# Kernel optimization log

Hardware: AMD Instinct MI355X
Metric: run time of the kernel (lower is better)

## Reference

```python
import jax, jax.numpy as jnp
import numpy as np
from jax.scipy.special import logsumexp

EPS = 0.1
MAX_ITER = 100
LOG_SHIFT = 1e-8


def setup_inputs() -> dict:
    key = jax.random.key(0)
    kx, ky = jax.random.split(key)
    x = jax.random.normal(kx, (4, 2048, 64), dtype=jnp.float32)
    y = jax.random.normal(ky, (4, 2048, 64), dtype=jnp.float32)
    return {"x": x, "y": y}


def _cost_matrix(x, y):
    # |x_i - y_j|^2 summed over features; for p=2 use the expanded quadratic form
    # to avoid materializing a [B, P1, P2, D] intermediate.
    x2 = jnp.sum(x * x, axis=-1)  # [B, P1]
    y2 = jnp.sum(y * y, axis=-1)  # [B, P2]
    xy = jnp.einsum('bpd,bqd->bpq', x, y)  # [B, P1, P2]
    return x2[:, :, None] + y2[:, None, :] - 2.0 * xy


def _M(C, u, v):
    # M_ij = (-C_ij + u_i + v_j) / eps
    return (-C + u[..., :, None] + v[..., None, :]) / EPS


def reference(x, y):
    C = _cost_matrix(x, y)  # [B, P1, P2]
    B, P1, P2 = C.shape
    mu = jnp.full((B, P1), 1.0 / P1, dtype=C.dtype)
    nu = jnp.full((B, P2), 1.0 / P2, dtype=C.dtype)
    log_mu = jnp.log(mu + LOG_SHIFT)
    log_nu = jnp.log(nu + LOG_SHIFT)

    def step(carry, _):
        u, v = carry
        u = EPS * (log_mu - logsumexp(_M(C, u, v), axis=-1)) + u
        # logsumexp of M^T over its last dim == logsumexp of M over axis -2
        v = EPS * (log_nu - logsumexp(_M(C, u, v), axis=-2)) + v
        return (u, v), None

    u0 = jnp.zeros_like(mu)
    v0 = jnp.zeros_like(nu)
    (u, v), _ = jax.lax.scan(step, (u0, v0), None, length=MAX_ITER)

    pi = jnp.exp(_M(C, u, v))  # transport plan [B, P1, P2]
    cost = jnp.sum(pi * C, axis=(-2, -1))  # [B], reduction='none'
    return cost, pi, C
```

## Files before the change

### kernel.cpp

```cpp
#include <hip/hip_runtime.h>
#include <hip/hip_bf16.h>
#include <math.h>


#define P 2048
#define D 64
#define B 4
#define ITERS 100
#define EPS 0.1f
#define KS 14.426950408889634f
#define EL2 0.06931471805599453f

#define EX2 __builtin_amdgcn_exp2f
#define LG2 __builtin_amdgcn_logf

__global__ __launch_bounds__(256) void cost_kernel(
    const float* __restrict__ X, const float* __restrict__ Y,
    float* __restrict__ C) {
  __shared__ float xs[64][65];
  __shared__ float ys[64][65];
  const int b = blockIdx.z;
  const int i0 = blockIdx.y * 64;
  const int j0 = blockIdx.x * 64;
  const float* Xb = X + ((size_t)b * P + i0) * D;
  const float* Yb = Y + ((size_t)b * P + j0) * D;
  const int t = threadIdx.x;
#pragma unroll
  for (int n = 0; n < 4; n++) {
    int e4 = t + n * 256;
    float4 xv = ((const float4*)Xb)[e4];
    float4 yv = ((const float4*)Yb)[e4];
    int r = e4 >> 4;
    int k = (e4 & 15) * 4;
    xs[r][k] = xv.x; xs[r][k + 1] = xv.y; xs[r][k + 2] = xv.z; xs[r][k + 3] = xv.w;
    ys[r][k] = yv.x; ys[r][k + 1] = yv.y; ys[r][k + 2] = yv.z; ys[r][k + 3] = yv.w;
  }
  __syncthreads();
  const int tx = t & 15;
  const int ty = t >> 4;
  float acc[4][4] = {};
#pragma unroll
  for (int k = 0; k < D; k++) {
    float a[4], bb[4];
#pragma unroll
    for (int r = 0; r < 4; r++) a[r] = xs[ty * 4 + r][k];
#pragma unroll
    for (int c = 0; c < 4; c++) bb[c] = ys[tx * 4 + c][k];
#pragma unroll
    for (int r = 0; r < 4; r++)
#pragma unroll
      for (int c = 0; c < 4; c++) {
        float d = a[r] - bb[c];
        acc[r][c] = fmaf(d, d, acc[r][c]);
      }
  }
#pragma unroll
  for (int r = 0; r < 4; r++) {
    float4 o = make_float4(acc[r][0], acc[r][1], acc[r][2], acc[r][3]);
    *(float4*)&C[((size_t)b * P + i0 + ty * 4 + r) * P + j0 + tx * 4] = o;
  }
}

__global__ __launch_bounds__(256, 3) void sweep8(
    const float* __restrict__ C, const float* __restrict__ vK,
    float* __restrict__ uK, float2* __restrict__ part, float elogK) {
  const int bid = blockIdx.x;
  const int rows0 = bid * 8;
  const int b = bid >> 8;
  const int kb = bid & 255;
  const int t = threadIdx.x;
  const int lane = t & 63;
  const int w = t >> 6;

  __shared__ float redm[4][8];
  __shared__ float reds[4][8];

  float vv[8];
  {
    const float4* vp = (const float4*)(vK + ((size_t)b << 11) + t * 8);
    float4 a = vp[0], q = vp[1];
    vv[0] = a.x; vv[1] = a.y; vv[2] = a.z; vv[3] = a.w;
    vv[4] = q.x; vv[5] = q.y; vv[6] = q.z; vv[7] = q.w;
  }

  float cK[8][8];
  {
    const float* Cb = C + (size_t)rows0 * P + t * 8;
#pragma unroll
    for (int r = 0; r < 8; r++) {
      float4 a = *(const float4*)(Cb + (size_t)r * P);
      float4 q = *(const float4*)(Cb + (size_t)r * P + 4);
      cK[r][0] = a.x * KS; cK[r][1] = a.y * KS; cK[r][2] = a.z * KS; cK[r][3] = a.w * KS;
      cK[r][4] = q.x * KS; cK[r][5] = q.y * KS; cK[r][6] = q.z * KS; cK[r][7] = q.w * KS;
    }
  }

  float bm[8];
#pragma unroll
  for (int r = 0; r < 8; r++) {
    float m = vv[0] - cK[r][0];
#pragma unroll
    for (int j = 1; j < 8; j++) m = fmaxf(m, vv[j] - cK[r][j]);
#pragma unroll
    for (int off = 32; off; off >>= 1) m = fmaxf(m, __shfl_xor(m, off));
    bm[r] = m;
  }
  if (lane == 0) {
#pragma unroll
    for (int r = 0; r < 8; r++) redm[w][r] = bm[r];
  }
  __syncthreads();
#pragma unroll
  for (int r = 0; r < 8; r++)
    bm[r] = fmaxf(fmaxf(redm[0][r], redm[1][r]),
                  fmaxf(redm[2][r], redm[3][r]));
  float ls[8];
#pragma unroll
  for (int r = 0; r < 8; r++) {
    float s = 0.f;
#pragma unroll
    for (int j = 0; j < 8; j++) s += EX2(vv[j] - cK[r][j] - bm[r]);
#pragma unroll
    for (int off = 32; off; off >>= 1) s += __shfl_xor(s, off);
    ls[r] = s;
  }
  if (lane == 0) {
#pragma unroll
    for (int r = 0; r < 8; r++) reds[w][r] = ls[r];
  }
  __syncthreads();
  float ur[8];
#pragma unroll
  for (int r = 0; r < 8; r++) {
    float S = (reds[0][r] + reds[1][r]) + (reds[2][r] + reds[3][r]);
    ur[r] = elogK - bm[r] - LG2(S);
  }
  if (t == 0) {
#pragma unroll
    for (int r = 0; r < 8; r++) uK[rows0 + r] = ur[r];
  }

  float4* p4 = (float4*)(part + (size_t)kb * (B * P) + ((size_t)b << 11) + t * 8);
#pragma unroll
  for (int i = 0; i < 4; i++) {
    float m0, s0, m1, s1;
    {
      const int cc = 2 * i;
      float z[8];
#pragma unroll
      for (int r = 0; r < 8; r++) z[r] = ur[r] - cK[r][cc];
      m0 = z[0];
#pragma unroll
      for (int r = 1; r < 8; r++) m0 = fmaxf(m0, z[r]);
      s0 = 0.f;
#pragma unroll
      for (int r = 0; r < 8; r++) s0 += EX2(z[r] - m0);
    }
    {
      const int cc = 2 * i + 1;
      float z[8];
#pragma unroll
      for (int r = 0; r < 8; r++) z[r] = ur[r] - cK[r][cc];
      m1 = z[0];
#pragma unroll
      for (int r = 1; r < 8; r++) m1 = fmaxf(m1, z[r]);
      s1 = 0.f;
#pragma unroll
      for (int r = 0; r < 8; r++) s1 += EX2(z[r] - m1);
    }
    p4[i] = make_float4(m0, s0, m1, s1);
  }
}

__global__ __launch_bounds__(256) void reduce_v3(
    const float2* __restrict__ part, float* __restrict__ vK, float elogK) {
  const int t = threadIdx.x;
  const int c = t & 15;
  const int seg = t >> 4;
  const int col = blockIdx.x * 16 + c;
  const float2* pk = part + (size_t)(seg * 16) * (B * P) + col;
  float m = -__builtin_inff();
  float s = 0.f;
#pragma unroll
  for (int i = 0; i < 16; i++) {
    float2 p = pk[(size_t)i * (B * P)];
    float M = fmaxf(m, p.x);
    s = s * EX2(m - M) + p.y * EX2(p.x - M);
    m = M;
  }
#pragma unroll
  for (int off = 16; off <= 32; off <<= 1) {
    float om = __shfl_xor(m, off);
    float os = __shfl_xor(s, off);
    float M = fmaxf(m, om);
    s = s * EX2(m - M) + os * EX2(om - M);
    m = M;
  }
  __shared__ float mm[4][16];
  __shared__ float ss[4][16];
  if ((t & 63) < 16) {
    mm[t >> 6][c] = m;
    ss[t >> 6][c] = s;
  }
  __syncthreads();
  if (t < 16) {
    float M0 = mm[0][t], S0 = ss[0][t];
#pragma unroll
    for (int k = 1; k < 4; k++) {
      float pm = mm[k][t], ps = ss[k][t];
      float M = fmaxf(M0, pm);
      S0 = S0 * EX2(M0 - M) + ps * EX2(pm - M);
      M0 = M;
    }
    vK[blockIdx.x * 16 + t] = elogK - M0 - LG2(S0);
  }
}

__global__ __launch_bounds__(256) void final_pi2(
    const float* __restrict__ C, const float* __restrict__ uK,
    const float* __restrict__ vK, float* __restrict__ pi,
    float* __restrict__ cost) {
  const int bid = blockIdx.x;
  const int rows0 = bid * 4;
  const int b = rows0 >> 11;
  const int t = threadIdx.x;
  const int lane = t & 63;
  const int w = t >> 6;

  float vv[8];
  {
    const float4* vp = (const float4*)(vK + ((size_t)b << 11) + t * 8);
    float4 a = vp[0], q = vp[1];
    vv[0] = a.x; vv[1] = a.y; vv[2] = a.z; vv[3] = a.w;
    vv[4] = q.x; vv[5] = q.y; vv[6] = q.z; vv[7] = q.w;
  }

  float acc = 0.f;
#pragma unroll
  for (int r = 0; r < 4; r++) {
    const int row = rows0 + r;
    const float u = uK[row];
    const float* cp = C + (size_t)row * P + t * 8;
    float4 a = *(const float4*)(cp);
    float4 q = *(const float4*)(cp + 4);
    float c[8] = {a.x, a.y, a.z, a.w, q.x, q.y, q.z, q.w};
    float p[8];
#pragma unroll
    for (int j = 0; j < 8; j++) {
      p[j] = EX2(u + vv[j] - c[j] * KS);
      acc = fmaf(p[j], c[j], acc);
    }
    float* pp = pi + (size_t)row * P + t * 8;
    *(float4*)(pp) = make_float4(p[0], p[1], p[2], p[3]);
    *(float4*)(pp + 4) = make_float4(p[4], p[5], p[6], p[7]);
  }
#pragma unroll
  for (int off = 32; off; off >>= 1) acc += __shfl_xor(acc, off);
  __shared__ float sa[4];
  if (lane == 0) sa[w] = acc;
  __syncthreads();
  if (t == 0) atomicAdd(cost + b, (sa[0] + sa[1]) + (sa[2] + sa[3]));
}

extern "C" void kernel_launch(void* const* d_in, const int* in_sizes, int n_in,
                              void* d_out, int out_size, void* d_ws,
                              size_t ws_size, hipStream_t stream) {
  const float* x = (const float*)d_in[0];
  const float* y = (const float*)d_in[1];
  float* out = (float*)d_out;
  float* cost = out;
  float* pi = out + 4;
  float* Cmat = out + 4 + (size_t)B * P * P;

  float2* part = (float2*)pi;
  float* vK = (float*)d_ws;
  float* uK = vK + B * P;

  hipMemsetAsync(vK, 0, B * P * sizeof(float), stream);
  hipMemsetAsync(cost, 0, 4 * sizeof(float), stream);

  dim3 cgrid(P / 64, P / 64, B);
  cost_kernel<<<cgrid, 256, 0, stream>>>(x, y, Cmat);

  const float elogK = log2f(1.0f / (float)P + 1e-8f);

  for (int it = 0; it < ITERS; it++) {
    sweep8<<<B * P / 8, 256, 0, stream>>>(Cmat, vK, uK, part, elogK);
    reduce_v3<<<B * P / 16, 256, 0, stream>>>(part, vK, elogK);
  }

  final_pi2<<<B * P / 4, 256, 0, stream>>>(Cmat, uK, vK, pi, cost);
}
```

Baseline: 2.713 ms.

## Use a transposed cost matrix so both Sinkhorn half-steps are row sweeps

Builds a second, transposed cost matrix in the pi output buffer. Each iteration now runs the same row-wise logsumexp kernel twice, once on C for u and once on C^T for v. This replaces the fused row sweep that wrote partial column (max, sum) pairs and the separate reduction kernel that merged them. Each iteration reads the full matrix twice instead of once plus a large partials write and read, and the sweep uses 4 rows per block with a higher occupancy hint.

```diff
diff --git a/kernel.cpp b/kernel.cpp
--- a/kernel.cpp
+++ b/kernel.cpp
@@ -9,7 +9,6 @@
 #define ITERS 100
 #define EPS 0.1f
 #define KS 14.426950408889634f
-#define EL2 0.06931471805599453f
 
 #define EX2 __builtin_amdgcn_exp2f
 #define LG2 __builtin_amdgcn_logf
@@ -61,158 +60,78 @@
   }
 }
 
-__global__ __launch_bounds__(256, 3) void sweep8(
-    const float* __restrict__ C, const float* __restrict__ vK,
-    float* __restrict__ uK, float2* __restrict__ part, float elogK) {
+__global__ __launch_bounds__(256, 4) void lse_sweep(
+    const float* __restrict__ mat, const float* __restrict__ vin,
+    float* __restrict__ vout, float elogK) {
   const int bid = blockIdx.x;
-  const int rows0 = bid * 8;
-  const int b = bid >> 8;
-  const int kb = bid & 255;
+  const int rows0 = bid * 4;
+  const int b = rows0 >> 11;
   const int t = threadIdx.x;
   const int lane = t & 63;
   const int w = t >> 6;
 
-  __shared__ float redm[4][8];
-  __shared__ float reds[4][8];
+  __shared__ float redm[4][4];
+  __shared__ float reds[4][4];
 
   float vv[8];
   {
-    const float4* vp = (const float4*)(vK + ((size_t)b << 11) + t * 8);
+    const float4* vp = (const float4*)(vin + ((size_t)b << 11) + t * 8);
     float4 a = vp[0], q = vp[1];
     vv[0] = a.x; vv[1] = a.y; vv[2] = a.z; vv[3] = a.w;
     vv[4] = q.x; vv[5] = q.y; vv[6] = q.z; vv[7] = q.w;
   }
 
-  float cK[8][8];
+  float za[4][8];
   {
-    const float* Cb = C + (size_t)rows0 * P + t * 8;
-#pragma unroll
-    for (int r = 0; r < 8; r++) {
-      float4 a = *(const float4*)(Cb + (size_t)r * P);
-      float4 q = *(const float4*)(Cb + (size_t)r * P + 4);
-      cK[r][0] = a.x * KS; cK[r][1] = a.y * KS; cK[r][2] = a.z * KS; cK[r][3] = a.w * KS;
-      cK[r][4] = q.x * KS; cK[r][5] = q.y * KS; cK[r][6] = q.z * KS; cK[r][7] = q.w * KS;
+    const float* Mb = mat + (size_t)rows0 * P + t * 8;
+#pragma unroll
+    for (int r = 0; r < 4; r++) {
+      float4 a = *(const float4*)(Mb + (size_t)r * P);
+      float4 q = *(const float4*)(Mb + (size_t)r * P + 4);
+      za[r][0] = fmaf(-KS, a.x, vv[0]); za[r][1] = fmaf(-KS, a.y, vv[1]);
+      za[r][2] = fmaf(-KS, a.z, vv[2]); za[r][3] = fmaf(-KS, a.w, vv[3]);
+      za[r][4] = fmaf(-KS, q.x, vv[4]); za[r][5] = fmaf(-KS, q.y, vv[5]);
+      za[r][6] = fmaf(-KS, q.z, vv[6]); za[r][7] = fmaf(-KS, q.w, vv[7]);
     }
   }
 
-  float bm[8];
-#pragma unroll
-  for (int r = 0; r < 8; r++) {
-    float m = vv[0] - cK[r][0];
-#pragma unroll
-    for (int j = 1; j < 8; j++) m = fmaxf(m, vv[j] - cK[r][j]);
+  float bm[4];
+#pragma unroll
+  for (int r = 0; r < 4; r++) {
+    float m = za[r][0];
+#pragma unroll
+    for (int j = 1; j < 8; j++) m = fmaxf(m, za[r][j]);
 #pragma unroll
     for (int off = 32; off; off >>= 1) m = fmaxf(m, __shfl_xor(m, off));
     bm[r] = m;
   }
   if (lane == 0) {
 #pragma unroll
-    for (int r = 0; r < 8; r++) redm[w][r] = bm[r];
-  }
-  __syncthreads();
-#pragma unroll
-  for (int r = 0; r < 8; r++)
+    for (int r = 0; r < 4; r++) redm[w][r] = bm[r];
+  }
+  __syncthreads();
+#pragma unroll
+  for (int r = 0; r < 4; r++)
     bm[r] = fmaxf(fmaxf(redm[0][r], redm[1][r]),
                   fmaxf(redm[2][r], redm[3][r]));
-  float ls[8];
-#pragma unroll
-  for (int r = 0; r < 8; r++) {
+
+#pragma unroll
+  for (int r = 0; r < 4; r++) {
     float s = 0.f;
 #pragma unroll
-    for (int j = 0; j < 8; j++) s += EX2(vv[j] - cK[r][j] - bm[r]);
+    for (int j = 0; j < 8; j++) s += EX2(za[r][j] - bm[r]);
 #pragma unroll
     for (int off = 32; off; off >>= 1) s += __shfl_xor(s, off);
-    ls[r] = s;
-  }
-  if (lane == 0) {
-#pragma unroll
-    for (int r = 0; r < 8; r++) reds[w][r] = ls[r];
-  }
-  __syncthreads();
-  float ur[8];
-#pragma unroll
-  for (int r = 0; r < 8; r++) {
-    float S = (reds[0][r] + reds[1][r]) + (reds[2][r] + reds[3][r]);
-    ur[r] = elogK - bm[r] - LG2(S);
-  }
+    if (lane == 0) reds[w][r] = s;
+  }
+  __syncthreads();
   if (t == 0) {
-#pragma unroll
-    for (int r = 0; r < 8; r++) uK[rows0 + r] = ur[r];
-  }
-
-  float4* p4 = (float4*)(part + (size_t)kb * (B * P) + ((size_t)b << 11) + t * 8);
-#pragma unroll
-  for (int i = 0; i < 4; i++) {
-    float m0, s0, m1, s1;
-    {
-      const int cc = 2 * i;
-      float z[8];
-#pragma unroll
-      for (int r = 0; r < 8; r++) z[r] = ur[r] - cK[r][cc];
-      m0 = z[0];
-#pragma unroll
-      for (int r = 1; r < 8; r++) m0 = fmaxf(m0, z[r]);
-      s0 = 0.f;
-#pragma unroll
-      for (int r = 0; r < 8; r++) s0 += EX2(z[r] - m0);
-    }
-    {
-      const int cc = 2 * i + 1;
-      float z[8];
-#pragma unroll
-      for (int r = 0; r < 8; r++) z[r] = ur[r] - cK[r][cc];
-      m1 = z[0];
-#pragma unroll
-      for (int r = 1; r < 8; r++) m1 = fmaxf(m1, z[r]);
-      s1 = 0.f;
-#pragma unroll
-      for (int r = 0; r < 8; r++) s1 += EX2(z[r] - m1);
-    }
-    p4[i] = make_float4(m0, s0, m1, s1);
-  }
-}
-
-__global__ __launch_bounds__(256) void reduce_v3(
-    const float2* __restrict__ part, float* __restrict__ vK, float elogK) {
-  const int t = threadIdx.x;
-  const int c = t & 15;
-  const int seg = t >> 4;
-  const int col = blockIdx.x * 16 + c;
-  const float2* pk = part + (size_t)(seg * 16) * (B * P) + col;
-  float m = -__builtin_inff();
-  float s = 0.f;
-#pragma unroll
-  for (int i = 0; i < 16; i++) {
-    float2 p = pk[(size_t)i * (B * P)];
-    float M = fmaxf(m, p.x);
-    s = s * EX2(m - M) + p.y * EX2(p.x - M);
-    m = M;
-  }
-#pragma unroll
-  for (int off = 16; off <= 32; off <<= 1) {
-    float om = __shfl_xor(m, off);
-    float os = __shfl_xor(s, off);
-    float M = fmaxf(m, om);
-    s = s * EX2(m - M) + os * EX2(om - M);
-    m = M;
-  }
-  __shared__ float mm[4][16];
-  __shared__ float ss[4][16];
-  if ((t & 63) < 16) {
-    mm[t >> 6][c] = m;
-    ss[t >> 6][c] = s;
-  }
-  __syncthreads();
-  if (t < 16) {
-    float M0 = mm[0][t], S0 = ss[0][t];
-#pragma unroll
-    for (int k = 1; k < 4; k++) {
-      float pm = mm[k][t], ps = ss[k][t];
-      float M = fmaxf(M0, pm);
-      S0 = S0 * EX2(M0 - M) + ps * EX2(pm - M);
-      M0 = M;
-    }
-    vK[blockIdx.x * 16 + t] = elogK - M0 - LG2(S0);
+    float4 o;
+    o.x = elogK - bm[0] - LG2((reds[0][0] + reds[1][0]) + (reds[2][0] + reds[3][0]));
+    o.y = elogK - bm[1] - LG2((reds[0][1] + reds[1][1]) + (reds[2][1] + reds[3][1]));
+    o.z = elogK - bm[2] - LG2((reds[0][2] + reds[1][2]) + (reds[2][2] + reds[3][2]));
+    o.w = elogK - bm[3] - LG2((reds[0][3] + reds[1][3]) + (reds[2][3] + reds[3][3]));
+    *(float4*)(vout + rows0) = o;
   }
 }
 
@@ -247,7 +166,7 @@
     float p[8];
 #pragma unroll
     for (int j = 0; j < 8; j++) {
-      p[j] = EX2(u + vv[j] - c[j] * KS);
+      p[j] = EX2(fmaf(-KS, c[j], u + vv[j]));
       acc = fmaf(p[j], c[j], acc);
     }
     float* pp = pi + (size_t)row * P + t * 8;
@@ -272,7 +191,7 @@
   float* pi = out + 4;
   float* Cmat = out + 4 + (size_t)B * P * P;
 
-  float2* part = (float2*)pi;
+  float* CT = pi;
   float* vK = (float*)d_ws;
   float* uK = vK + B * P;
 
@@ -281,12 +200,13 @@
 
   dim3 cgrid(P / 64, P / 64, B);
   cost_kernel<<<cgrid, 256, 0, stream>>>(x, y, Cmat);
+  cost_kernel<<<cgrid, 256, 0, stream>>>(y, x, CT);
 
   const float elogK = log2f(1.0f / (float)P + 1e-8f);
 
   for (int it = 0; it < ITERS; it++) {
-    sweep8<<<B * P / 8, 256, 0, stream>>>(Cmat, vK, uK, part, elogK);
-    reduce_v3<<<B * P / 16, 256, 0, stream>>>(part, vK, elogK);
+    lse_sweep<<<B * P / 4, 256, 0, stream>>>(Cmat, vK, uK, elogK);
+    lse_sweep<<<B * P / 4, 256, 0, stream>>>(CT, uK, vK, elogK);
   }
 
   final_pi2<<<B * P / 4, 256, 0, stream>>>(Cmat, uK, vK, pi, cost);
```

New measurement: 2.781 ms. 1.02x slower.
